# Kernel optimization log

Hardware: AMD Instinct MI355X
Metric: run time of the kernel (lower is better)

## Reference

```python
import jax, jax.numpy as jnp
import numpy as np

N = 8          # num_tasks (PHQ-8)
D_EMB = 64     # task_embed_dim
HID = 128      # hidden_dim
L = 2          # num_gat_layers
H = 4          # num_heads
B = 16384      # batch size

CLUSTERS = {'core_depression': [0, 1, 5], 'cognitive': [6, 7], 'somatic': [2, 3, 4]}
CROSS = [(0, 6), (0, 7), (1, 6), (1, 7), (5, 6), (5, 7), (0, 2), (0, 3), (1, 2), (1, 3), (1, 4), (6, 2), (7, 3)]


def build_graph():
    adj = np.eye(N, dtype=np.int32)
    et = np.zeros((N, N), dtype=np.int32)
    for idxs in CLUSTERS.values():
        for i in idxs:
            for j in idxs:
                adj[i, j] = 1
                if i != j:
                    et[i, j] = 1
    for i, j in CROSS:
        adj[i, j] = 1
        adj[j, i] = 1
        et[i, j] = 2
        et[j, i] = 2
    return adj, et


def setup_inputs() -> dict:
    key = jax.random.key(0)
    ks = jax.random.split(key, 10)
    adj, et = build_graph()
    s = 0.05
    return {
        'shared_embedding': jax.random.normal(ks[0], (B, HID), dtype=jnp.float32),
        'task_embeddings': jax.random.normal(ks[1], (N, D_EMB), dtype=jnp.float32) * s,
        'W_in': jax.random.normal(ks[2], (HID, D_EMB), dtype=jnp.float32) * s,
        'b_in': jnp.zeros((HID,), dtype=jnp.float32),
        'W_heads': jax.random.normal(ks[3], (L, H, HID, HID), dtype=jnp.float32) * s,
        'a_heads': jax.random.normal(ks[4], (L, H, 2 * HID), dtype=jnp.float32) * s,
        'out_W': jax.random.normal(ks[5], (L, HID, H * HID), dtype=jnp.float32) * s,
        'out_b': jnp.zeros((L, HID), dtype=jnp.float32),
        'ln_scale': jnp.ones((L, HID), dtype=jnp.float32),
        'ln_bias': jnp.zeros((L, HID), dtype=jnp.float32),
        'omega_intra': jnp.asarray(1.0, dtype=jnp.float32),
        'omega_cross': jnp.asarray(0.6, dtype=jnp.float32),
        'adj': jnp.asarray(adj),
        'edge_types': jnp.asarray(et),
    }


def reference(shared_embedding, task_embeddings, W_in, b_in, W_heads, a_heads,
              out_W, out_b, ln_scale, ln_bias, omega_intra, omega_cross, adj, edge_types):
    adjf = adj.astype(jnp.float32)
    # learnable edge weights: intra-cluster omega_intra, cross-cluster omega_cross, zero off-edge
    ew = jnp.ones_like(adjf)
    ew = jnp.where(edge_types == 1, omega_intra, ew)
    ew = jnp.where(edge_types == 2, omega_cross, ew)
    ew = ew * adjf  # [N, N]

    b = shared_embedding.shape[0]
    h_task = task_embeddings @ W_in.T + b_in          # [N, HID]
    h = h_task[None, :, :] + shared_embedding[:, None, :]  # [B, N, HID]

    n_layers = W_heads.shape[0]
    for l in range(n_layers):
        # per-head projection: Linear(y = x W^T), W_heads[l]: [H, out, in]
        Wh = jnp.einsum('bnf,hgf->bhng', h, W_heads[l])  # [B, H, N, F]
        f = Wh.shape[-1]
        a_src = a_heads[l][:, :f]   # [H, F]
        a_dst = a_heads[l][:, f:]   # [H, F]
        # concat-based additive score decomposed into two dot products
        ei = jnp.einsum('bhnf,hf->bhn', Wh, a_src)
        ej = jnp.einsum('bhnf,hf->bhn', Wh, a_dst)
        e = jax.nn.leaky_relu(ei[:, :, :, None] + ej[:, :, None, :], 0.2)  # [B,H,N,N]
        att = jnp.where(adjf[None, None] > 0, e, jnp.float32(-9e15))
        # faithful to original: masked entries multiplied by (zero) edge weights -> 0 logits
        att = att * ew[None, None]
        att = jax.nn.softmax(att, axis=-1)
        hp = jax.nn.elu(jnp.einsum('bhnm,bhmf->bhnf', att, Wh))  # [B,H,N,F]
        hcat = jnp.moveaxis(hp, 1, 2).reshape(b, hp.shape[2], -1)  # [B,N,H*F]
        gout = hcat @ out_W[l].T + out_b[l]  # [B,N,HID]
        # residual + layernorm
        x = h + gout
        mu = x.mean(-1, keepdims=True)
        var = x.var(-1, keepdims=True)
        h = (x - mu) / jnp.sqrt(var + 1e-5) * ln_scale[l] + ln_bias[l]
    return h, ew
```

## Files before the change

### kernel.cpp

```cpp
#include <hip/hip_runtime.h>
#include <stdint.h>

typedef __attribute__((ext_vector_type(8))) short bf16x8;
typedef __attribute__((ext_vector_type(4))) float f32x4;
typedef unsigned long long ull;

typedef uint4 uint4_a __attribute__((may_alias));
typedef ull ull_a __attribute__((may_alias));
typedef bf16x8 bf16x8_a __attribute__((may_alias));

#define LGKM0() __builtin_amdgcn_s_waitcnt(0xc07f)
#define MFMA16(a, b, c) __builtin_amdgcn_mfma_f32_16x16x32_bf16((a), (b), (c), 0, 0, 0)

__device__ __forceinline__ unsigned f2bf(float x) {
    unsigned u = __float_as_uint(x);
    return (u + 0x7fffu + ((u >> 16) & 1u)) >> 16;
}
__device__ __forceinline__ float bf2f(short s) {
    return __uint_as_float(((unsigned)(unsigned short)s) << 16);
}
__device__ __forceinline__ ull pack4(f32x4 v) {
    return (ull)f2bf(v.x) | ((ull)f2bf(v.y) << 16) | ((ull)f2bf(v.z) << 32) | ((ull)f2bf(v.w) << 48);
}

__global__ void gat_prep(const float* __restrict__ te, const float* __restrict__ W_in,
                         const float* __restrict__ b_in, const float* __restrict__ W_heads,
                         const float* __restrict__ a_heads, const float* __restrict__ om_i,
                         const float* __restrict__ om_c, const int* __restrict__ adj,
                         const int* __restrict__ et, const float* __restrict__ out_W,
                         unsigned short* __restrict__ wsW1, unsigned short* __restrict__ wsW2,
                         unsigned short* __restrict__ wsWsd, float* __restrict__ wsHt,
                         float* __restrict__ wsEw, float* __restrict__ eout) {
    const int gid = blockIdx.x, tid = threadIdx.x;
    if (gid < 1024) {
        int idx = gid * 256 + tid;
        if (idx < 131072) wsW1[idx] = (unsigned short)f2bf(W_heads[idx]);
        else wsW2[idx - 131072] = (unsigned short)f2bf(out_W[idx - 131072]);
    } else if (gid < 1028) {
        int idx = (gid - 1024) * 256 + tid;
        int n = idx >> 7, o = idx & 127;
        float s = b_in[o];
        for (int f = 0; f < 64; ++f) s += te[n * 64 + f] * W_in[o * 64 + f];
        wsHt[idx] = s;
    } else if (gid < 1044) {
        int idx = (gid - 1028) * 256 + tid;
        int l = idx >> 11, p = (idx >> 7) & 15, f = idx & 127;
        float s = 0.f;
        if (p < 8) {
            int hh = p >> 1, ss = p & 1;
            const float* a = a_heads + (l * 4 + hh) * 256 + ss * 128;
            const float* Wb = W_heads + (l * 4 + hh) * 16384;
            for (int g = 0; g < 128; ++g) s += a[g] * Wb[g * 128 + f];
        }
        wsWsd[idx] = (unsigned short)f2bf(s);
    } else {
        if (tid < 64) {
            float v = 0.f;
            if (adj[tid]) {
                int t = et[tid];
                v = (t == 1) ? om_i[0] : ((t == 2) ? om_c[0] : 1.0f);
            }
            wsEw[tid] = v;
            eout[tid] = v;
        }
    }
}

__device__ __forceinline__ void load_chunk(int chunk, int tid,
                                           const unsigned short* __restrict__ wsW1,
                                           const unsigned short* __restrict__ wsW2, uint4* pf) {
    const int l = chunk >> 3, h = (chunk >> 1) & 3;
    const int r = tid >> 2, part = tid & 3;
    const unsigned short* src = (chunk & 1) ? (wsW2 + ((l << 7) + r) * 512 + (h << 7) + part * 32)
                                            : (wsW1 + (((l << 2) + h) * 128 + r) * 128 + part * 32);
#pragma unroll
    for (int k = 0; k < 4; ++k) pf[k] = *(const uint4_a*)(src + 8 * k);
}

__global__ __launch_bounds__(512, 1) void gat_main(
    const float* __restrict__ shared_emb, const float* __restrict__ out_b,
    const float* __restrict__ ln_s, const float* __restrict__ ln_b,
    const unsigned short* __restrict__ wsW1, const unsigned short* __restrict__ wsW2,
    const unsigned short* __restrict__ wsWsd, const float* __restrict__ wsHt,
    const float* __restrict__ wsEw, float* __restrict__ out) {
    __shared__ __align__(16) unsigned short sW[128 * 136];
    __shared__ __align__(16) unsigned short sScr[8][5120];
    __shared__ __align__(16) float sE[8][32][8];
    __shared__ __align__(16) unsigned short sAtt[8][32][8];

    const int tid = threadIdx.x;
    const int w = tid >> 6, lane = tid & 63, q = lane >> 4, c = lane & 15;
    const long wrow0 = (long)blockIdx.x * 256 + (long)w * 32;

    float ewr[8];
#pragma unroll
    for (int m = 0; m < 8; ++m) ewr[m] = wsEw[(lane & 7) * 8 + m];

    bf16x8 xf[2][4];
#pragma unroll
    for (int mt = 0; mt < 2; ++mt) {
        const long row = wrow0 + 16 * mt + c;
        const size_t b = (size_t)(row >> 3);
        const int t = (int)(row & 7);
#pragma unroll
        for (int kk = 0; kk < 4; ++kk) {
            const int f0 = 32 * kk + 8 * q;
            const float4 s0 = *(const float4*)(shared_emb + b * 128 + f0);
            const float4 s1 = *(const float4*)(shared_emb + b * 128 + f0 + 4);
            const float4 h0 = *(const float4*)(wsHt + t * 128 + f0);
            const float4 h1 = *(const float4*)(wsHt + t * 128 + f0 + 4);
            float v[8] = {s0.x + h0.x, s0.y + h0.y, s0.z + h0.z, s0.w + h0.w,
                          s1.x + h1.x, s1.y + h1.y, s1.z + h1.z, s1.w + h1.w};
            bf16x8 r;
#pragma unroll
            for (int j = 0; j < 8; ++j) r[j] = (short)f2bf(v[j]);
            xf[mt][kk] = r;
        }
    }

    f32x4 gacc[8][2];
    uint4 pf[4];
    load_chunk(0, tid, wsW1, wsW2, pf);

    for (int chunk = 0; chunk < 16; ++chunk) {
        const int l = chunk >> 3, h = (chunk >> 1) & 3, isW2 = chunk & 1;
        {
            const int r = tid >> 2, part = tid & 3;
            unsigned short* dst = &sW[r * 136 + part * 32];
#pragma unroll
            for (int k = 0; k < 4; ++k) *(uint4_a*)(dst + 8 * k) = pf[k];
        }
        if (chunk < 15) load_chunk(chunk + 1, tid, wsW1, wsW2, pf);
        __syncthreads();

        if (!isW2) {
            if (h == 0) {
                const f32x4 z4 = {0.f, 0.f, 0.f, 0.f};
#pragma unroll
                for (int ot = 0; ot < 8; ++ot)
#pragma unroll
                    for (int nt = 0; nt < 2; ++nt) gacc[ot][nt] = z4;
                f32x4 e[2] = {z4, z4};
#pragma unroll
                for (int kk = 0; kk < 4; ++kk) {
                    bf16x8 bw = *(const bf16x8_a*)(wsWsd + ((l << 4) + c) * 128 + 32 * kk + 8 * q);
#pragma unroll
                    for (int mt = 0; mt < 2; ++mt) e[mt] = MFMA16(xf[mt][kk], bw, e[mt]);
                }
                if (c < 8) {
#pragma unroll
                    for (int mt = 0; mt < 2; ++mt)
#pragma unroll
                        for (int r = 0; r < 4; ++r) sE[w][16 * mt + 4 * q + r][c] = e[mt][r];
                }
                LGKM0();
            }
            if (lane < 32) {
                const int r = lane, eb = r & 24;
                const float ei = sE[w][r][2 * h];
                float lgt[8];
#pragma unroll
                for (int m = 0; m < 8; ++m) {
                    float s = ei + sE[w][eb + m][2 * h + 1];
                    s = s > 0.f ? s : 0.2f * s;
                    lgt[m] = s * ewr[m];
                }
                float mx = lgt[0];
#pragma unroll
                for (int m = 1; m < 8; ++m) mx = fmaxf(mx, lgt[m]);
                float p[8], sum = 0.f;
#pragma unroll
                for (int m = 0; m < 8; ++m) {
                    p[m] = __expf(lgt[m] - mx);
                    sum += p[m];
                }
                const float inv = 1.0f / sum;
                uint4 av;
                av.x = f2bf(p[0] * inv) | (f2bf(p[1] * inv) << 16);
                av.y = f2bf(p[2] * inv) | (f2bf(p[3] * inv) << 16);
                av.z = f2bf(p[4] * inv) | (f2bf(p[5] * inv) << 16);
                av.w = f2bf(p[6] * inv) | (f2bf(p[7] * inv) << 16);
                *(uint4_a*)&sAtt[w][r][0] = av;
            }
            f32x4 acc[16];
            {
                const f32x4 z4 = {0.f, 0.f, 0.f, 0.f};
#pragma unroll
                for (int i = 0; i < 16; ++i) acc[i] = z4;
            }
#pragma unroll
            for (int kk = 0; kk < 4; ++kk)
#pragma unroll
                for (int gt = 0; gt < 8; ++gt) {
                    bf16x8 bw = *(const bf16x8_a*)&sW[(16 * gt + c) * 136 + 32 * kk + 8 * q];
#pragma unroll
                    for (int mt = 0; mt < 2; ++mt)
                        acc[mt * 8 + gt] = MFMA16(xf[mt][kk], bw, acc[mt * 8 + gt]);
                }
            LGKM0();
#pragma unroll
            for (int gt = 0; gt < 8; ++gt)
#pragma unroll
                for (int mt = 0; mt < 2; ++mt)
                    *(ull_a*)&sScr[w][(16 * gt + c) * 40 + 16 * mt + 4 * q] = pack4(acc[mt * 8 + gt]);
            LGKM0();
            bf16x8 bat[2];
#pragma unroll
            for (int nt = 0; nt < 2; ++nt) {
                const int n = 16 * nt + c;
                bf16x8 zb;
#pragma unroll
                for (int j = 0; j < 8; ++j) zb[j] = 0;
                bat[nt] = (q == 2 * nt + (c >> 3)) ? *(const bf16x8_a*)&sAtt[w][n][0] : zb;
            }
            {
                const f32x4 z4 = {0.f, 0.f, 0.f, 0.f};
#pragma unroll
                for (int i = 0; i < 16; ++i) acc[i] = z4;
            }
#pragma unroll
            for (int ct = 0; ct < 8; ++ct) {
                bf16x8 a0 = *(const bf16x8_a*)&sScr[w][(16 * ct + c) * 40 + 8 * q];
#pragma unroll
                for (int nt = 0; nt < 2; ++nt)
                    acc[ct * 2 + nt] = MFMA16(a0, bat[nt], acc[ct * 2 + nt]);
            }
            LGKM0();
#pragma unroll
            for (int ct = 0; ct < 8; ++ct)
#pragma unroll
                for (int nt = 0; nt < 2; ++nt) {
                    f32x4 v = acc[ct * 2 + nt];
#pragma unroll
                    for (int j = 0; j < 4; ++j) {
                        float x = v[j];
                        v[j] = x > 0.f ? x : (__expf(x) - 1.f);
                    }
                    *(ull_a*)&sScr[w][(16 * nt + c) * 136 + 16 * ct + 4 * q] = pack4(v);
                }
            LGKM0();
        } else {
#pragma unroll
            for (int kk = 0; kk < 4; ++kk) {
                bf16x8 bh[2];
#pragma unroll
                for (int nt = 0; nt < 2; ++nt)
                    bh[nt] = *(const bf16x8_a*)&sScr[w][(16 * nt + c) * 136 + 32 * kk + 8 * q];
#pragma unroll
                for (int ot = 0; ot < 8; ++ot) {
                    bf16x8 aw = *(const bf16x8_a*)&sW[(16 * ot + c) * 136 + 32 * kk + 8 * q];
#pragma unroll
                    for (int nt = 0; nt < 2; ++nt) gacc[ot][nt] = MFMA16(aw, bh[nt], gacc[ot][nt]);
                }
            }
            if (h == 3) {
                LGKM0();
#pragma unroll
                for (int ot = 0; ot < 8; ++ot)
#pragma unroll
                    for (int nt = 0; nt < 2; ++nt)
                        *(ull_a*)&sScr[w][(16 * nt + c) * 136 + 16 * ot + 4 * q] = pack4(gacc[ot][nt]);
                LGKM0();
                const float* ob = out_b + l * 128;
                float sum[2] = {0.f, 0.f}, ssq[2] = {0.f, 0.f};
#pragma unroll
                for (int mt = 0; mt < 2; ++mt)
#pragma unroll
                    for (int kk = 0; kk < 4; ++kk) {
                        bf16x8 g8 = *(const bf16x8_a*)&sScr[w][(16 * mt + c) * 136 + 32 * kk + 8 * q];
                        bf16x8 x8 = xf[mt][kk];
                        const int f0 = 32 * kk + 8 * q;
#pragma unroll
                        for (int j = 0; j < 8; ++j) {
                            float x = bf2f(g8[j]) + bf2f(x8[j]) + ob[f0 + j];
                            sum[mt] += x;
                            ssq[mt] += x * x;
                        }
                    }
                float mu[2], rs[2];
#pragma unroll
                for (int mt = 0; mt < 2; ++mt) {
                    sum[mt] += __shfl_xor(sum[mt], 16);
                    sum[mt] += __shfl_xor(sum[mt], 32);
                    ssq[mt] += __shfl_xor(ssq[mt], 16);
                    ssq[mt] += __shfl_xor(ssq[mt], 32);
                    mu[mt] = sum[mt] * (1.0f / 128.0f);
                    float var = ssq[mt] * (1.0f / 128.0f) - mu[mt] * mu[mt];
                    rs[mt] = rsqrtf(var + 1e-5f);
                }
                const float* lsc = ln_s + l * 128;
                const float* lbi = ln_b + l * 128;
#pragma unroll
                for (int mt = 0; mt < 2; ++mt) {
                    const long row = wrow0 + 16 * mt + c;
#pragma unroll
                    for (int kk = 0; kk < 4; ++kk) {
                        bf16x8 g8 = *(const bf16x8_a*)&sScr[w][(16 * mt + c) * 136 + 32 * kk + 8 * q];
                        bf16x8 x8 = xf[mt][kk];
                        const int f0 = 32 * kk + 8 * q;
                        float y[8];
#pragma unroll
                        for (int j = 0; j < 8; ++j) {
                            float x = bf2f(g8[j]) + bf2f(x8[j]) + ob[f0 + j];
                            y[j] = (x - mu[mt]) * rs[mt] * lsc[f0 + j] + lbi[f0 + j];
                        }
                        if (l == 0) {
                            bf16x8 r;
#pragma unroll
                            for (int j = 0; j < 8; ++j) r[j] = (short)f2bf(y[j]);
                            xf[mt][kk] = r;
                        } else {
                            float4 o0 = {y[0], y[1], y[2], y[3]};
                            float4 o1 = {y[4], y[5], y[6], y[7]};
                            *(float4*)(out + (size_t)row * 128 + f0) = o0;
                            *(float4*)(out + (size_t)row * 128 + f0 + 4) = o1;
                        }
                    }
                }
            }
        }
        __syncthreads();
    }
}

extern "C" void kernel_launch(void* const* d_in, const int* in_sizes, int n_in, void* d_out,
                              int out_size, void* d_ws, size_t ws_size, hipStream_t stream) {
    const float* shared_emb = (const float*)d_in[0];
    const float* te = (const float*)d_in[1];
    const float* W_in = (const float*)d_in[2];
    const float* b_in = (const float*)d_in[3];
    const float* W_heads = (const float*)d_in[4];
    const float* a_heads = (const float*)d_in[5];
    const float* out_W = (const float*)d_in[6];
    const float* out_b = (const float*)d_in[7];
    const float* ln_s = (const float*)d_in[8];
    const float* ln_b = (const float*)d_in[9];
    const float* om_i = (const float*)d_in[10];
    const float* om_c = (const float*)d_in[11];
    const int* adj = (const int*)d_in[12];
    const int* et = (const int*)d_in[13];
    float* out = (float*)d_out;

    unsigned short* wsW1 = (unsigned short*)d_ws;
    unsigned short* wsW2 = wsW1 + 131072;
    unsigned short* wsWsd = wsW2 + 131072;
    float* wsHt = (float*)((char*)d_ws + 532480);
    float* wsEw = wsHt + 1024;

    float* eout = out + (out_size - 64);

    gat_prep<<<1045, 256, 0, stream>>>(te, W_in, b_in, W_heads, a_heads, om_i, om_c, adj, et,
                                       out_W, wsW1, wsW2, wsWsd, wsHt, wsEw, eout);

    const int B = in_sizes[0] / 128;
    const int grid = (B * 8) / 256;
    gat_main<<<grid, 512, 0, stream>>>(shared_emb, out_b, ln_s, ln_b, wsW1, wsW2, wsWsd, wsHt,
                                       wsEw, out);
}
```

Before: 360.8 us.

## Double-buffer weight chunks in LDS and split W1 GEMM to target two waves/EU

Doubles the shared-memory weight tile so consecutive chunks alternate buffers. It also splits the per-head Wh GEMM into two halves of 8 accumulators instead of 16, to cut register pressure. The launch bound changes from one block per CU to an explicit waves_per_eu(2,2), which trades a tighter register budget for more latency hiding. Doubling LDS usage (sW grows by about 34KB) may cap occupancy, so the extra waves might not materialize.

```diff
diff --git a/kernel.cpp b/kernel.cpp
--- a/kernel.cpp
+++ b/kernel.cpp
@@ -77,13 +77,13 @@
     for (int k = 0; k < 4; ++k) pf[k] = *(const uint4_a*)(src + 8 * k);
 }
 
-__global__ __launch_bounds__(512, 1) void gat_main(
+__global__ __launch_bounds__(512) __attribute__((amdgpu_waves_per_eu(2, 2))) void gat_main(
     const float* __restrict__ shared_emb, const float* __restrict__ out_b,
     const float* __restrict__ ln_s, const float* __restrict__ ln_b,
     const unsigned short* __restrict__ wsW1, const unsigned short* __restrict__ wsW2,
     const unsigned short* __restrict__ wsWsd, const float* __restrict__ wsHt,
     const float* __restrict__ wsEw, float* __restrict__ out) {
-    __shared__ __align__(16) unsigned short sW[128 * 136];
+    __shared__ __align__(16) unsigned short sW[2][128 * 136];
     __shared__ __align__(16) unsigned short sScr[8][5120];
     __shared__ __align__(16) float sE[8][32][8];
     __shared__ __align__(16) unsigned short sAtt[8][32][8];
@@ -91,6 +91,7 @@
     const int tid = threadIdx.x;
     const int w = tid >> 6, lane = tid & 63, q = lane >> 4, c = lane & 15;
     const long wrow0 = (long)blockIdx.x * 256 + (long)w * 32;
+    const f32x4 z4 = {0.f, 0.f, 0.f, 0.f};
 
     float ewr[8];
 #pragma unroll
@@ -126,7 +127,7 @@
         const int l = chunk >> 3, h = (chunk >> 1) & 3, isW2 = chunk & 1;
         {
             const int r = tid >> 2, part = tid & 3;
-            unsigned short* dst = &sW[r * 136 + part * 32];
+            unsigned short* dst = &sW[chunk & 1][r * 136 + part * 32];
 #pragma unroll
             for (int k = 0; k < 4; ++k) *(uint4_a*)(dst + 8 * k) = pf[k];
         }
@@ -135,7 +136,6 @@
 
         if (!isW2) {
             if (h == 0) {
-                const f32x4 z4 = {0.f, 0.f, 0.f, 0.f};
 #pragma unroll
                 for (int ot = 0; ot < 8; ++ot)
 #pragma unroll
@@ -182,27 +182,28 @@
                 av.w = f2bf(p[6] * inv) | (f2bf(p[7] * inv) << 16);
                 *(uint4_a*)&sAtt[w][r][0] = av;
             }
-            f32x4 acc[16];
-            {
-                const f32x4 z4 = {0.f, 0.f, 0.f, 0.f};
-#pragma unroll
-                for (int i = 0; i < 16; ++i) acc[i] = z4;
-            }
-#pragma unroll
-            for (int kk = 0; kk < 4; ++kk)
-#pragma unroll
-                for (int gt = 0; gt < 8; ++gt) {
-                    bf16x8 bw = *(const bf16x8_a*)&sW[(16 * gt + c) * 136 + 32 * kk + 8 * q];
+            LGKM0();
+#pragma unroll
+            for (int half = 0; half < 2; ++half) {
+                f32x4 acc[8];
+#pragma unroll
+                for (int i = 0; i < 8; ++i) acc[i] = z4;
+#pragma unroll
+                for (int kk = 0; kk < 4; ++kk)
+#pragma unroll
+                    for (int g4 = 0; g4 < 4; ++g4) {
+                        const int gt = half * 4 + g4;
+                        bf16x8 bw = *(const bf16x8_a*)&sW[chunk & 1][(16 * gt + c) * 136 + 32 * kk + 8 * q];
+                        acc[g4 * 2] = MFMA16(xf[0][kk], bw, acc[g4 * 2]);
+                        acc[g4 * 2 + 1] = MFMA16(xf[1][kk], bw, acc[g4 * 2 + 1]);
+                    }
+#pragma unroll
+                for (int g4 = 0; g4 < 4; ++g4)
 #pragma unroll
                     for (int mt = 0; mt < 2; ++mt)
-                        acc[mt * 8 + gt] = MFMA16(xf[mt][kk], bw, acc[mt * 8 + gt]);
-                }
-            LGKM0();
-#pragma unroll
-            for (int gt = 0; gt < 8; ++gt)
-#pragma unroll
-                for (int mt = 0; mt < 2; ++mt)
-                    *(ull_a*)&sScr[w][(16 * gt + c) * 40 + 16 * mt + 4 * q] = pack4(acc[mt * 8 + gt]);
+                        *(ull_a*)&sScr[w][(16 * (half * 4 + g4) + c) * 40 + 16 * mt + 4 * q] =
+                            pack4(acc[g4 * 2 + mt]);
+            }
             LGKM0();
             bf16x8 bat[2];
 #pragma unroll
@@ -213,24 +214,22 @@
                 for (int j = 0; j < 8; ++j) zb[j] = 0;
                 bat[nt] = (q == 2 * nt + (c >> 3)) ? *(const bf16x8_a*)&sAtt[w][n][0] : zb;
             }
-            {
-                const f32x4 z4 = {0.f, 0.f, 0.f, 0.f};
-#pragma unroll
-                for (int i = 0; i < 16; ++i) acc[i] = z4;
-            }
+            f32x4 macc[16];
+#pragma unroll
+            for (int i = 0; i < 16; ++i) macc[i] = z4;
 #pragma unroll
             for (int ct = 0; ct < 8; ++ct) {
                 bf16x8 a0 = *(const bf16x8_a*)&sScr[w][(16 * ct + c) * 40 + 8 * q];
 #pragma unroll
                 for (int nt = 0; nt < 2; ++nt)
-                    acc[ct * 2 + nt] = MFMA16(a0, bat[nt], acc[ct * 2 + nt]);
+                    macc[ct * 2 + nt] = MFMA16(a0, bat[nt], macc[ct * 2 + nt]);
             }
             LGKM0();
 #pragma unroll
             for (int ct = 0; ct < 8; ++ct)
 #pragma unroll
                 for (int nt = 0; nt < 2; ++nt) {
-                    f32x4 v = acc[ct * 2 + nt];
+                    f32x4 v = macc[ct * 2 + nt];
 #pragma unroll
                     for (int j = 0; j < 4; ++j) {
                         float x = v[j];
@@ -248,7 +247,7 @@
                     bh[nt] = *(const bf16x8_a*)&sScr[w][(16 * nt + c) * 136 + 32 * kk + 8 * q];
 #pragma unroll
                 for (int ot = 0; ot < 8; ++ot) {
-                    bf16x8 aw = *(const bf16x8_a*)&sW[(16 * ot + c) * 136 + 32 * kk + 8 * q];
+                    bf16x8 aw = *(const bf16x8_a*)&sW[chunk & 1][(16 * ot + c) * 136 + 32 * kk + 8 * q];
 #pragma unroll
                     for (int nt = 0; nt < 2; ++nt) gacc[ot][nt] = MFMA16(aw, bh[nt], gacc[ot][nt]);
                 }
```

Measured after the change: 381.9 us. 1.06x slower.
